# Performance work log

Measured on AMD Instinct MI355X. Metric: run time of the kernel, lower is better.

Reference implementation:

```python
import jax, jax.numpy as jnp
import numpy as np

N_NODES = 50000
N_EDGES = 800000
NODE_FEAT = 176
EDGE_FEAT = 4
HIDDEN = 64
LAYERS = 4
LN_EPS = 1e-5


def setup_inputs() -> dict:
    key = jax.random.key(0)
    ks = jax.random.split(key, 20)
    H, H2, Hh = HIDDEN, HIDDEN * 2, HIDDEN // 2
    inp = {
        "x": jax.random.normal(ks[0], (N_NODES, NODE_FEAT), jnp.float32),
        "edge_index": jax.random.randint(ks[1], (2, N_EDGES), 0, N_NODES, jnp.int64),
        "edge_attr": jax.random.normal(ks[2], (N_EDGES, EDGE_FEAT), jnp.float32),
        # input projection
        "in_w": jax.random.normal(ks[3], (NODE_FEAT, H), jnp.float32) * 0.05,
        "in_b": jnp.zeros((H,), jnp.float32),
        # per-layer GINEConv params (stacked over LAYERS)
        "edge_w": jax.random.normal(ks[4], (LAYERS, EDGE_FEAT, H), jnp.float32) * 0.1,
        "edge_b": jnp.zeros((LAYERS, H), jnp.float32),
        "mlp_w1": jax.random.normal(ks[5], (LAYERS, H, H2), jnp.float32) * 0.05,
        "mlp_b1": jnp.zeros((LAYERS, H2), jnp.float32),
        "mlp_w2": jax.random.normal(ks[6], (LAYERS, H2, H), jnp.float32) * 0.05,
        "mlp_b2": jnp.zeros((LAYERS, H), jnp.float32),
        "ln_g": jnp.ones((LAYERS, H), jnp.float32),
        "ln_b": jnp.zeros((LAYERS, H), jnp.float32),
        "reg_w1": jax.random.normal(ks[7], (H, Hh), jnp.float32) * 0.1,
        "reg_b1": jnp.zeros((Hh,), jnp.float32),
        "reg_w2": jax.random.normal(ks[8], (Hh, 1), jnp.float32) * 0.1,
        "reg_b2": jnp.zeros((1,), jnp.float32),
    }
    return inp


def _layernorm(z, g, b):
    mu = jnp.mean(z, axis=-1, keepdims=True)
    var = jnp.mean((z - mu) ** 2, axis=-1, keepdims=True)
    return g * (z - mu) * jax.lax.rsqrt(var + LN_EPS) + b


def reference(x, edge_index, edge_attr, in_w, in_b, edge_w, edge_b,
              mlp_w1, mlp_b1, mlp_w2, mlp_b2, ln_g, ln_b,
              reg_w1, reg_b1, reg_w2, reg_b2):
    src, dst = edge_index[0], edge_index[1]
    h = x @ in_w + in_b  # [N, H]
    for l in range(LAYERS):
        e = edge_attr @ edge_w[l] + edge_b[l]              # [E, H] edge projection
        msg = jax.nn.relu(h[src] + e)                      # gather + relu
        aggr = jax.ops.segment_sum(msg, dst, num_segments=h.shape[0])  # scatter-add
        z = h + aggr                                       # (1+eps)*x_i + aggr, eps=0
        z = jax.nn.relu(z @ mlp_w1[l] + mlp_b1[l]) @ mlp_w2[l] + mlp_b2[l]
        h = jax.nn.relu(_layernorm(z, ln_g[l], ln_b[l]))
    g = jnp.sum(h, axis=0)                                 # global_add_pool, single graph
    out = jax.nn.relu(g @ reg_w1 + reg_b1) @ reg_w2 + reg_b2
    return out.squeeze()
```

## Files before the change

kernel.cpp:

```cpp
#include <hip/hip_runtime.h>

#define N_NODES 50000
#define N_EDGES 800000
#define NODE_FEAT 176
#define HIDDEN 64
#define LN_EPS 1e-5f
#define SCAN_NB 49

typedef short bf16x8 __attribute__((ext_vector_type(8)));
typedef float f32x4 __attribute__((ext_vector_type(4)));
typedef long long ll2 __attribute__((ext_vector_type(2)));

__device__ __forceinline__ unsigned short f2bf(float f) {
    unsigned int u = __float_as_uint(f);
    u += 0x7FFFu + ((u >> 16) & 1u);
    return (unsigned short)(u >> 16);
}
__device__ __forceinline__ int pack2(float lo, float hi) {
    return (int)(((unsigned)f2bf(hi) << 16) | (unsigned)f2bf(lo));
}
__device__ __forceinline__ float bf2f(unsigned short s) {
    return __uint_as_float(((unsigned int)s) << 16);
}

#if __has_builtin(__builtin_amdgcn_cvt_pk_fp8_f32) && __has_builtin(__builtin_amdgcn_cvt_f32_fp8)
#define HW_FP8 1
#endif

__device__ __forceinline__ unsigned char f2fp8(float f) {
#ifdef HW_FP8
    return (unsigned char)(__builtin_amdgcn_cvt_pk_fp8_f32(f, f, 0, false) & 0xff);
#else
    unsigned u = __float_as_uint(f);
    unsigned s = (u >> 24) & 0x80u;
    float a = fabsf(f);
    if (a >= 448.f) return (unsigned char)(s | 0x7E);
    if (a < 0.0078125f) {
        int m = (int)fmaf(a, 512.0f, 0.5f);
        return (unsigned char)(s | (m > 7 ? 7 : m));
    }
    unsigned au = u & 0x7fffffffu;
    au += 0x7ffffu + ((au >> 20) & 1u);
    int e8 = (int)(au >> 23) - 120;
    if (e8 <= 0) {
        int m = (int)fmaf(__uint_as_float(au), 512.0f, 0.5f);
        return (unsigned char)(s | (m > 7 ? 7 : m));
    }
    if (e8 > 15) return (unsigned char)(s | 0x7E);
    return (unsigned char)(s | (e8 << 3) | ((au >> 20) & 7));
#endif
}
__device__ __forceinline__ float fp82f(int b) {
#ifdef HW_FP8
    return __builtin_amdgcn_cvt_f32_fp8(b & 0xff, 0);
#else
    int s = (b >> 7) & 1, e = (b >> 3) & 15, m = b & 7;
    float v = e ? __uint_as_float(((unsigned)(e + 120) << 23) | ((unsigned)m << 20))
                : (float)m * 0.001953125f;
    return s ? -v : v;
#endif
}

__device__ __forceinline__ float wave_sum64(float v) {
#pragma unroll
    for (int o = 32; o > 0; o >>= 1) v += __shfl_xor(v, o);
    return v;
}
__device__ __forceinline__ float sum16(float v) {
#pragma unroll
    for (int o = 8; o > 0; o >>= 1) v += __shfl_xor(v, o);
    return v;
}

__global__ __launch_bounds__(256) void k_wprep(const float* __restrict__ in_w,
                                               const float* __restrict__ w1,
                                               const float* __restrict__ w2,
                                               unsigned short* __restrict__ fin,
                                               unsigned short* __restrict__ f1,
                                               unsigned short* __restrict__ f2,
                                               int* __restrict__ cnt) {
    int t = blockIdx.x * 256 + threadIdx.x;
    if (t < N_NODES) cnt[t] = 0;
    if (t < 12288) {
        int e = t;
        int r = e & 7, lane = (e >> 3) & 63, j = (e >> 9) & 3, s = e >> 11;
        int k = s * 32 + ((lane >> 4) << 3) + r;
        int n = (j << 4) + (lane & 15);
        fin[e] = (k < NODE_FEAT) ? f2bf(in_w[k * 64 + n]) : (unsigned short)0;
    } else if (t < 12288 + 32768) {
        int e = t - 12288;
        int L = e >> 13, e2 = e & 8191;
        int r = e2 & 7, lane = (e2 >> 3) & 63, j = (e2 >> 9) & 7, s = (e2 >> 12) & 1;
        int k = s * 32 + ((lane >> 4) << 3) + r;
        int n = (j << 4) + (lane & 15);
        f1[e] = f2bf(w1[L * 8192 + k * 128 + n]);
    } else if (t < 12288 + 32768 + 32768) {
        int e = t - 45056;
        int L = e >> 13, e2 = e & 8191;
        int r = e2 & 7, lane = (e2 >> 3) & 63, j = (e2 >> 9) & 3, s = (e2 >> 11) & 3;
        int k = s * 32 + ((lane >> 4) << 3) + r;
        int n = (j << 4) + (lane & 15);
        f2[e] = f2bf(w2[L * 8192 + k * 64 + n]);
    }
}

__global__ __launch_bounds__(256) void k_inproj_mfma(const float* __restrict__ x,
                                                     const unsigned short* __restrict__ wfrag,
                                                     const float* __restrict__ in_b,
                                                     unsigned short* __restrict__ hb,
                                                     unsigned char* __restrict__ hf8) {
    __shared__ unsigned short lw[12288];
    const int tid = threadIdx.x;
    {
        const bf16x8* src = (const bf16x8*)wfrag;
        bf16x8* dst = (bf16x8*)lw;
        for (int i = tid; i < 1536; i += 256) dst[i] = src[i];
    }
    __syncthreads();
    const int wv = tid >> 6, lane = tid & 63;
    const int lrow = lane & 15, lgrp = lane >> 4;
    float ib[4];
#pragma unroll
    for (int j = 0; j < 4; ++j) ib[j] = in_b[16 * j + lrow];
    const int nwaves = gridDim.x * 4;
    for (int tile = blockIdx.x * 4 + wv; tile < 3125; tile += nwaves) {
        const int m0 = tile * 16;
        f32x4 acc[4];
#pragma unroll
        for (int j = 0; j < 4; ++j) acc[j] = (f32x4){ib[j], ib[j], ib[j], ib[j]};
#pragma unroll
        for (int s = 0; s < 6; ++s) {
            const int kbase = s * 32 + lgrp * 8;
            bf16x8 a;
            if (kbase < NODE_FEAT) {
                const float* p = x + (size_t)(m0 + lrow) * NODE_FEAT + kbase;
                float4 fa = *(const float4*)p;
                float4 fb = *(const float4*)(p + 4);
                a[0] = (short)f2bf(fa.x); a[1] = (short)f2bf(fa.y);
                a[2] = (short)f2bf(fa.z); a[3] = (short)f2bf(fa.w);
                a[4] = (short)f2bf(fb.x); a[5] = (short)f2bf(fb.y);
                a[6] = (short)f2bf(fb.z); a[7] = (short)f2bf(fb.w);
            } else {
                a = (bf16x8){0, 0, 0, 0, 0, 0, 0, 0};
            }
#pragma unroll
            for (int j = 0; j < 4; ++j) {
                bf16x8 b = *(const bf16x8*)&lw[((s * 4 + j) * 64 + lane) * 8];
                acc[j] = __builtin_amdgcn_mfma_f32_16x16x32_bf16(a, b, acc[j], 0, 0, 0);
            }
        }
#pragma unroll
        for (int j = 0; j < 4; ++j) {
            const int col = 16 * j + lrow;
#pragma unroll
            for (int r = 0; r < 4; ++r) {
                const int node = m0 + lgrp * 4 + r;
                float v = acc[j][r];
                __builtin_nontemporal_store(f2bf(v), &hb[(size_t)node * 64 + col]);
                hf8[(size_t)node * 64 + col] = f2fp8(v);
            }
        }
    }
}

__global__ __launch_bounds__(256) void k_hist(const int* __restrict__ ei,
                                              int* __restrict__ cnt,
                                              int* __restrict__ erank) {
    const int tid = blockIdx.x * 256 + threadIdx.x;
#pragma unroll
    for (int k = 0; k < 6; ++k) {
        int e = tid + k * 131072;
        erank[e] = atomicAdd(&cnt[ei[N_EDGES + e]], 1);
    }
    {
        int e = tid + 6 * 131072;
        if (e < N_EDGES) erank[e] = atomicAdd(&cnt[ei[N_EDGES + e]], 1);
    }
}

__global__ __launch_bounds__(256) void k_scan_part(const int* __restrict__ cnt,
                                                   int* __restrict__ blksum) {
    const int b = blockIdx.x, t = threadIdx.x;
    const int base = b * 1024 + t * 4;
    int s = 0;
#pragma unroll
    for (int i = 0; i < 4; ++i) {
        int idx = base + i;
        if (idx < N_NODES) s += cnt[idx];
    }
#pragma unroll
    for (int o = 32; o > 0; o >>= 1) s += __shfl_xor(s, o);
    __shared__ int wt[4];
    if ((t & 63) == 0) wt[t >> 6] = s;
    __syncthreads();
    if (t == 0) blksum[b] = wt[0] + wt[1] + wt[2] + wt[3];
}

__global__ __launch_bounds__(256) void k_scan_add(const int* __restrict__ cnt,
                                                  const int* __restrict__ blksum,
                                                  int* __restrict__ row_ptr) {
    const int b = blockIdx.x, t = threadIdx.x;
    __shared__ int boff_s;
    if (t < 64) {
        int v = (t < SCAN_NB) ? blksum[t] : 0;
        int incl = v;
#pragma unroll
        for (int o = 1; o < 64; o <<= 1) {
            int u = __shfl_up(incl, o);
            if (t >= o) incl += u;
        }
        if (t == b) boff_s = incl - v;
        if (b == 0 && t == 63) row_ptr[N_NODES] = incl;
    }
    __syncthreads();
    const int base = b * 1024 + t * 4;
    int c[4];
    int tsum = 0;
#pragma unroll
    for (int i = 0; i < 4; ++i) {
        int idx = base + i;
        c[i] = (idx < N_NODES) ? cnt[idx] : 0;
        tsum += c[i];
    }
    int incl = tsum;
#pragma unroll
    for (int o = 1; o < 64; o <<= 1) {
        int u = __shfl_up(incl, o);
        if ((t & 63) >= o) incl += u;
    }
    __shared__ int wt[4];
    const int wv = t >> 6;
    if ((t & 63) == 63) wt[wv] = incl;
    __syncthreads();
    int run = boff_s + (incl - tsum);
    for (int w = 0; w < wv; ++w) run += wt[w];
#pragma unroll
    for (int i = 0; i < 4; ++i) {
        int idx = base + i;
        if (idx < N_NODES) row_ptr[idx] = run;
        run += c[i];
    }
}

__global__ __launch_bounds__(256) void k_scatter(const int* __restrict__ ei,
                                                 const float4* __restrict__ ea,
                                                 const int* __restrict__ row_ptr,
                                                 const int* __restrict__ erank,
                                                 int4* __restrict__ rec) {
    int e = blockIdx.x * 256 + threadIdx.x;
    if (e >= N_EDGES) return;
    int d = ei[N_EDGES + e];
    float4 a = ea[e];
    int4 r;
    r.x = pack2(a.x, a.y);
    r.y = pack2(a.z, a.w);
    r.z = ei[e];
    r.w = 0;
    rec[row_ptr[d] + erank[e]] = r;
}

__global__ __launch_bounds__(256) void k_aggr(const unsigned short* __restrict__ hb_in,
                                              const unsigned char* __restrict__ hf8_in,
                                              unsigned short* __restrict__ zb,
                                              const int* __restrict__ row_ptr,
                                              const int4* __restrict__ rec,
                                              const float* __restrict__ ew,
                                              const float* __restrict__ eb) {
    const int wv = threadIdx.x >> 6, lane = threadIdx.x & 63;
    const int node = blockIdx.x * 4 + wv;
    const float ew0 = ew[0 * 64 + lane], ew1 = ew[1 * 64 + lane];
    const float ew2 = ew[2 * 64 + lane], ew3 = ew[3 * 64 + lane];
    const float ebl = eb[lane];
    const int beg = __builtin_amdgcn_readfirstlane(row_ptr[node]);
    const int end = __builtin_amdgcn_readfirstlane(row_ptr[node + 1]);
    float acc = bf2f(__builtin_nontemporal_load(&hb_in[(size_t)node * 64 + lane]));
    const int nb = (end - beg) >> 3;
    int i = beg;
    ll2 ra[8];
    if (nb > 0) {
#pragma unroll
        for (int t = 0; t < 8; ++t)
            ra[t] = __builtin_nontemporal_load((const ll2*)(rec + i + t));
    }
    for (int k = 0; k < nb; ++k) {
        ll2 rb[8];
        if (k + 1 < nb) {
#pragma unroll
            for (int t = 0; t < 8; ++t)
                rb[t] = __builtin_nontemporal_load((const ll2*)(rec + i + 8 + t));
        }
        int d0[8], d1[8], sx[8];
#pragma unroll
        for (int t = 0; t < 8; ++t) {
            d0[t] = __builtin_amdgcn_readfirstlane((int)(ra[t][0] & 0xffffffffLL));
            d1[t] = __builtin_amdgcn_readfirstlane((int)(ra[t][0] >> 32));
            sx[t] = __builtin_amdgcn_readfirstlane((int)(ra[t][1] & 0xffffffffLL));
        }
        float gg[8];
#pragma unroll
        for (int t = 0; t < 8; ++t)
            gg[t] = fp82f(hf8_in[((size_t)sx[t] << 6) + lane]);
#pragma unroll
        for (int t = 0; t < 8; ++t) {
            float a0 = __uint_as_float((unsigned)d0[t] << 16);
            float a1 = __uint_as_float((unsigned)d0[t] & 0xffff0000u);
            float a2 = __uint_as_float((unsigned)d1[t] << 16);
            float a3 = __uint_as_float((unsigned)d1[t] & 0xffff0000u);
            float v = fmaf(a0, ew0, fmaf(a1, ew1, fmaf(a2, ew2, fmaf(a3, ew3, ebl))));
            acc += fmaxf(v + gg[t], 0.0f);
        }
        if (k + 1 < nb) {
#pragma unroll
            for (int t = 0; t < 8; ++t) ra[t] = rb[t];
        }
        i += 8;
    }
    if (i < end) {
        const int n = end - i;
        int d0[8], d1[8], sx[8];
#pragma unroll
        for (int t = 0; t < 8; ++t) {
            int idx = i + ((t < n) ? t : (n - 1));
            ll2 r = __builtin_nontemporal_load((const ll2*)(rec + idx));
            d0[t] = __builtin_amdgcn_readfirstlane((int)(r[0] & 0xffffffffLL));
            d1[t] = __builtin_amdgcn_readfirstlane((int)(r[0] >> 32));
            sx[t] = __builtin_amdgcn_readfirstlane((int)(r[1] & 0xffffffffLL));
        }
        float gg[8];
#pragma unroll
        for (int t = 0; t < 8; ++t)
            gg[t] = fp82f(hf8_in[((size_t)sx[t] << 6) + lane]);
#pragma unroll
        for (int t = 0; t < 8; ++t) {
            float m = (t < n) ? 1.0f : 0.0f;
            float a0 = __uint_as_float((unsigned)d0[t] << 16);
            float a1 = __uint_as_float((unsigned)d0[t] & 0xffff0000u);
            float a2 = __uint_as_float((unsigned)d1[t] << 16);
            float a3 = __uint_as_float((unsigned)d1[t] & 0xffff0000u);
            float v = fmaf(a0, ew0, fmaf(a1, ew1, fmaf(a2, ew2, fmaf(a3, ew3, ebl))));
            acc += m * fmaxf(v + gg[t], 0.0f);
        }
    }
    __builtin_nontemporal_store(f2bf(acc), &zb[(size_t)node * 64 + lane]);
}

__global__ __launch_bounds__(256) void k_mlp_mfma(const unsigned short* __restrict__ zb,
                                                  unsigned short* __restrict__ hb_out,
                                                  unsigned char* __restrict__ hf8_out,
                                                  const unsigned short* __restrict__ f1,
                                                  const unsigned short* __restrict__ f2,
                                                  const float* __restrict__ b1,
                                                  const float* __restrict__ b2,
                                                  const float* __restrict__ lng,
                                                  const float* __restrict__ lnb) {
    __shared__ unsigned short w1f[8192];
    __shared__ unsigned short w2f[8192];
    __shared__ unsigned short z1s[4][2048];
    const int tid = threadIdx.x;
    {
        const bf16x8* s1 = (const bf16x8*)f1;
        const bf16x8* s2 = (const bf16x8*)f2;
        bf16x8* d1 = (bf16x8*)w1f;
        bf16x8* d2 = (bf16x8*)w2f;
        for (int i = tid; i < 1024; i += 256) { d1[i] = s1[i]; d2[i] = s2[i]; }
    }
    __syncthreads();
    const int wv = tid >> 6, lane = tid & 63;
    const int lrow = lane & 15, lgrp = lane >> 4;
    unsigned short* zs = z1s[wv];
    float bb1[8], bb2[4], g4[4], be4[4];
#pragma unroll
    for (int j = 0; j < 8; ++j) bb1[j] = b1[16 * j + lrow];
#pragma unroll
    for (int j = 0; j < 4; ++j) {
        bb2[j] = b2[16 * j + lrow];
        g4[j] = lng[16 * j + lrow];
        be4[j] = lnb[16 * j + lrow];
    }
    const int nwaves = gridDim.x * 4;
    for (int tile = blockIdx.x * 4 + wv; tile < 3125; tile += nwaves) {
        const int m0 = tile * 16;
        f32x4 acc1[8];
#pragma unroll
        for (int j = 0; j < 8; ++j) acc1[j] = (f32x4){bb1[j], bb1[j], bb1[j], bb1[j]};
#pragma unroll
        for (int s = 0; s < 2; ++s) {
            const int kbase = s * 32 + lgrp * 8;
            bf16x8 a = *(const bf16x8*)&zb[(size_t)(m0 + lrow) * 64 + kbase];
#pragma unroll
            for (int j = 0; j < 8; ++j) {
                bf16x8 b = *(const bf16x8*)&w1f[((s * 8 + j) * 64 + lane) * 8];
                acc1[j] = __builtin_amdgcn_mfma_f32_16x16x32_bf16(a, b, acc1[j], 0, 0, 0);
            }
        }
#pragma unroll
        for (int j = 0; j < 8; ++j) {
            const int col = 16 * j + lrow;
#pragma unroll
            for (int r = 0; r < 4; ++r) {
                const int row = lgrp * 4 + r;
                const int idx = (row * 128 + col) ^ ((row & 7) << 3);
                zs[idx] = f2bf(fmaxf(acc1[j][r], 0.0f));
            }
        }
        f32x4 acc2[4];
#pragma unroll
        for (int j = 0; j < 4; ++j) acc2[j] = (f32x4){bb2[j], bb2[j], bb2[j], bb2[j]};
#pragma unroll
        for (int s = 0; s < 4; ++s) {
            const int kbase = s * 32 + lgrp * 8;
            const int idx = (lrow * 128 + kbase) ^ ((lrow & 7) << 3);
            bf16x8 a = *(const bf16x8*)&zs[idx];
#pragma unroll
            for (int j = 0; j < 4; ++j) {
                bf16x8 b = *(const bf16x8*)&w2f[((s * 4 + j) * 64 + lane) * 8];
                acc2[j] = __builtin_amdgcn_mfma_f32_16x16x32_bf16(a, b, acc2[j], 0, 0, 0);
            }
        }
#pragma unroll
        for (int r = 0; r < 4; ++r) {
            float sum = acc2[0][r] + acc2[1][r] + acc2[2][r] + acc2[3][r];
            sum = sum16(sum);
            const float mu = sum * (1.0f / 64.0f);
            float sq = 0.0f;
#pragma unroll
            for (int j = 0; j < 4; ++j) {
                float d = acc2[j][r] - mu;
                sq = fmaf(d, d, sq);
            }
            sq = sum16(sq);
            const float rstd = rsqrtf(sq * (1.0f / 64.0f) + LN_EPS);
            const int node = m0 + lgrp * 4 + r;
#pragma unroll
            for (int j = 0; j < 4; ++j) {
                const int col = 16 * j + lrow;
                float d = acc2[j][r] - mu;
                float hn = fmaxf(fmaf(g4[j] * d, rstd, be4[j]), 0.0f);
                __builtin_nontemporal_store(f2bf(hn), &hb_out[(size_t)node * 64 + col]);
                hf8_out[(size_t)node * 64 + col] = f2fp8(hn);
            }
        }
    }
}

__global__ __launch_bounds__(256) void k_pool(const unsigned short* __restrict__ hb,
                                              float* __restrict__ gpart) {
    __shared__ float red[256];
    const int tid = threadIdx.x;
    const int lane = tid & 63;
    float part = 0.0f;
    for (int i = blockIdx.x * 4 + (tid >> 6); i < N_NODES; i += gridDim.x * 4)
        part += bf2f(hb[(size_t)i * 64 + lane]);
    red[tid] = part;
    __syncthreads();
    if (tid < 64) {
        gpart[blockIdx.x * 64 + tid] = red[tid] + red[tid + 64] + red[tid + 128] + red[tid + 192];
    }
}

__global__ __launch_bounds__(64) void k_reg(const float* __restrict__ gpart,
                                            const float* __restrict__ w1,
                                            const float* __restrict__ b1,
                                            const float* __restrict__ w2,
                                            const float* __restrict__ b2,
                                            float* __restrict__ out) {
    const int j = threadIdx.x;
    float gj = 0.0f;
    for (int b = 0; b < 256; ++b) gj += gpart[b * 64 + j];
    __shared__ float gs[64];
    gs[j] = gj;
    __syncthreads();
    const int jm = j & 31;
    float acc = b1[jm];
#pragma unroll 8
    for (int k = 0; k < 64; ++k) {
        float gk = gs[k];
        acc = fmaf(gk, w1[k * 32 + jm], acc);
    }
    float contrib = (j < 32) ? fmaxf(acc, 0.0f) * w2[jm] : 0.0f;
    float s = wave_sum64(contrib);
    if (j == 0) out[0] = s + b2[0];
}

extern "C" void kernel_launch(void* const* d_in, const int* in_sizes, int n_in,
                              void* d_out, int out_size, void* d_ws, size_t ws_size,
                              hipStream_t stream) {
    const float* x      = (const float*)d_in[0];
    const int*   ei     = (const int*)d_in[1];
    const float* ea     = (const float*)d_in[2];
    const float* in_w   = (const float*)d_in[3];
    const float* in_b   = (const float*)d_in[4];
    const float* edge_w = (const float*)d_in[5];
    const float* edge_b = (const float*)d_in[6];
    const float* mlp_w1 = (const float*)d_in[7];
    const float* mlp_b1 = (const float*)d_in[8];
    const float* mlp_w2 = (const float*)d_in[9];
    const float* mlp_b2 = (const float*)d_in[10];
    const float* ln_g   = (const float*)d_in[11];
    const float* ln_b   = (const float*)d_in[12];
    const float* reg_w1 = (const float*)d_in[13];
    const float* reg_b1 = (const float*)d_in[14];
    const float* reg_w2 = (const float*)d_in[15];
    const float* reg_b2 = (const float*)d_in[16];

    char* ws = (char*)d_ws;
    unsigned short* hb0     = (unsigned short*)ws; ws += (size_t)N_NODES * 64 * 2;
    unsigned short* hb1     = (unsigned short*)ws; ws += (size_t)N_NODES * 64 * 2;
    unsigned short* zb      = (unsigned short*)ws; ws += (size_t)N_NODES * 64 * 2;
    unsigned char*  hf8_0   = (unsigned char*)ws;  ws += (size_t)N_NODES * 64;
    unsigned char*  hf8_1   = (unsigned char*)ws;  ws += (size_t)N_NODES * 64;
    int4*           rec     = (int4*)ws;           ws += (size_t)N_EDGES * 16;
    unsigned short* fin     = (unsigned short*)ws; ws += 12288 * 2;
    unsigned short* f1      = (unsigned short*)ws; ws += 32768 * 2;
    unsigned short* f2      = (unsigned short*)ws; ws += 32768 * 2;
    int*            erank   = (int*)ws;            ws += (size_t)N_EDGES * 4;
    int*            row_ptr = (int*)ws;            ws += (size_t)(N_NODES + 1) * 4;
    int*            cnt     = (int*)ws;            ws += (size_t)N_NODES * 4;
    int*            blksum  = (int*)ws;            ws += SCAN_NB * 4;
    float*          gpart   = (float*)ws;          ws += 256 * 64 * 4;
    float*          outf    = (float*)d_out;

    const int eb_blocks = (N_EDGES + 255) / 256;

    k_wprep<<<304, 256, 0, stream>>>(in_w, mlp_w1, mlp_w2, fin, f1, f2, cnt);

    k_hist<<<512, 256, 0, stream>>>(ei, cnt, erank);
    k_scan_part<<<SCAN_NB, 256, 0, stream>>>(cnt, blksum);
    k_scan_add<<<SCAN_NB, 256, 0, stream>>>(cnt, blksum, row_ptr);
    k_scatter<<<eb_blocks, 256, 0, stream>>>(ei, (const float4*)ea, row_ptr, erank, rec);

    k_inproj_mfma<<<512, 256, 0, stream>>>(x, fin, in_b, hb0, hf8_0);

    unsigned short* hbA = hb0;
    unsigned short* hbB = hb1;
    unsigned char*  hfA = hf8_0;
    unsigned char*  hfB = hf8_1;
    for (int l = 0; l < 4; ++l) {
        k_aggr<<<N_NODES / 4, 256, 0, stream>>>(hbA, hfA, zb, row_ptr, rec,
                                                edge_w + l * 4 * 64,
                                                edge_b + l * 64);
        k_mlp_mfma<<<768, 256, 0, stream>>>(zb, hbB, hfB,
                                            f1 + l * 8192, f2 + l * 8192,
                                            mlp_b1 + l * 128, mlp_b2 + l * 64,
                                            ln_g + l * 64, ln_b + l * 64);
        unsigned short* tb = hbA; hbA = hbB; hbB = tb;
        unsigned char*  tf = hfA; hfA = hfB; hfB = tf;
    }

    k_pool<<<256, 256, 0, stream>>>(hbA, gpart);
    k_reg<<<1, 64, 0, stream>>>(gpart, reg_w1, reg_b1, reg_w2, reg_b2, outf);
}
```

Measured before the change: 284.3 us.

## Replace global-atomic CSR build with per-block LDS histograms and offset matrix

The edge bucketing by destination moves from global atomics (histogram plus per-edge rank) to 64 blocks, each building LDS histograms over four node ranges for its edge chunk. A 64xN count matrix is scanned to produce per-block write offsets, and a second pass scatters records using LDS atomics for the local rank. This removes contended global atomics and the erank array. In exchange, only 64 blocks run, each edge chunk is scanned eight times in total, and the scan kernels now read and write large count and offset matrices.

```diff
diff --git a/kernel.cpp b/kernel.cpp
--- a/kernel.cpp
+++ b/kernel.cpp
@@ -6,6 +6,9 @@
 #define HIDDEN 64
 #define LN_EPS 1e-5f
 #define SCAN_NB 49
+#define NBC 64
+#define CHUNK 12500
+#define RNG 12500
 
 typedef short bf16x8 __attribute__((ext_vector_type(8)));
 typedef float f32x4 __attribute__((ext_vector_type(4)));
@@ -77,10 +80,8 @@
                                                const float* __restrict__ w2,
                                                unsigned short* __restrict__ fin,
                                                unsigned short* __restrict__ f1,
-                                               unsigned short* __restrict__ f2,
-                                               int* __restrict__ cnt) {
+                                               unsigned short* __restrict__ f2) {
     int t = blockIdx.x * 256 + threadIdx.x;
-    if (t < N_NODES) cnt[t] = 0;
     if (t < 12288) {
         int e = t;
         int r = e & 7, lane = (e >> 3) & 63, j = (e >> 9) & 3, s = e >> 11;
@@ -163,31 +164,47 @@
     }
 }
 
-__global__ __launch_bounds__(256) void k_hist(const int* __restrict__ ei,
-                                              int* __restrict__ cnt,
-                                              int* __restrict__ erank) {
-    const int tid = blockIdx.x * 256 + threadIdx.x;
-#pragma unroll
-    for (int k = 0; k < 6; ++k) {
-        int e = tid + k * 131072;
-        erank[e] = atomicAdd(&cnt[ei[N_EDGES + e]], 1);
-    }
-    {
-        int e = tid + 6 * 131072;
-        if (e < N_EDGES) erank[e] = atomicAdd(&cnt[ei[N_EDGES + e]], 1);
-    }
-}
-
-__global__ __launch_bounds__(256) void k_scan_part(const int* __restrict__ cnt,
+__global__ __launch_bounds__(256) void k_cnt(const int* __restrict__ ei,
+                                             unsigned short* __restrict__ cmat) {
+    __shared__ int h[RNG];
+    const int b = blockIdx.x, t = threadIdx.x;
+    const int e0 = b * CHUNK;
+    unsigned short* crow = cmat + (size_t)b * N_NODES;
+    for (int r = 0; r < 4; ++r) {
+        const int lo = r * RNG;
+        for (int i = t; i < RNG; i += 256) h[i] = 0;
+        __syncthreads();
+        for (int i = t; i < CHUNK; i += 256) {
+            int d = ei[N_EDGES + e0 + i];
+            unsigned dr = (unsigned)(d - lo);
+            if (dr < (unsigned)RNG) atomicAdd(&h[dr], 1);
+        }
+        __syncthreads();
+        for (int i = t; i < RNG; i += 256) crow[lo + i] = (unsigned short)h[i];
+        __syncthreads();
+    }
+}
+
+__global__ __launch_bounds__(256) void k_scan_part(const unsigned short* __restrict__ cmat,
+                                                   int* __restrict__ cnttot,
                                                    int* __restrict__ blksum) {
     const int b = blockIdx.x, t = threadIdx.x;
     const int base = b * 1024 + t * 4;
-    int s = 0;
+    int c[4] = {0, 0, 0, 0};
+    for (int bb = 0; bb < NBC; ++bb) {
+        const unsigned short* row = cmat + (size_t)bb * N_NODES;
+#pragma unroll
+        for (int i = 0; i < 4; ++i) {
+            int idx = base + i;
+            if (idx < N_NODES) c[i] += row[idx];
+        }
+    }
 #pragma unroll
     for (int i = 0; i < 4; ++i) {
         int idx = base + i;
-        if (idx < N_NODES) s += cnt[idx];
-    }
+        if (idx < N_NODES) cnttot[idx] = c[i];
+    }
+    int s = c[0] + c[1] + c[2] + c[3];
 #pragma unroll
     for (int o = 32; o > 0; o >>= 1) s += __shfl_xor(s, o);
     __shared__ int wt[4];
@@ -196,9 +213,11 @@
     if (t == 0) blksum[b] = wt[0] + wt[1] + wt[2] + wt[3];
 }
 
-__global__ __launch_bounds__(256) void k_scan_add(const int* __restrict__ cnt,
+__global__ __launch_bounds__(256) void k_scan_add(const int* __restrict__ cnttot,
                                                   const int* __restrict__ blksum,
-                                                  int* __restrict__ row_ptr) {
+                                                  const unsigned short* __restrict__ cmat,
+                                                  int* __restrict__ row_ptr,
+                                                  int* __restrict__ omat) {
     const int b = blockIdx.x, t = threadIdx.x;
     __shared__ int boff_s;
     if (t < 64) {
@@ -219,7 +238,7 @@
 #pragma unroll
     for (int i = 0; i < 4; ++i) {
         int idx = base + i;
-        c[i] = (idx < N_NODES) ? cnt[idx] : 0;
+        c[i] = (idx < N_NODES) ? cnttot[idx] : 0;
         tsum += c[i];
     }
     int incl = tsum;
@@ -234,29 +253,57 @@
     __syncthreads();
     int run = boff_s + (incl - tsum);
     for (int w = 0; w < wv; ++w) run += wt[w];
+    int rp[4];
 #pragma unroll
     for (int i = 0; i < 4; ++i) {
         int idx = base + i;
+        rp[i] = run;
         if (idx < N_NODES) row_ptr[idx] = run;
         run += c[i];
     }
-}
-
-__global__ __launch_bounds__(256) void k_scatter(const int* __restrict__ ei,
-                                                 const float4* __restrict__ ea,
-                                                 const int* __restrict__ row_ptr,
-                                                 const int* __restrict__ erank,
-                                                 int4* __restrict__ rec) {
-    int e = blockIdx.x * 256 + threadIdx.x;
-    if (e >= N_EDGES) return;
-    int d = ei[N_EDGES + e];
-    float4 a = ea[e];
-    int4 r;
-    r.x = pack2(a.x, a.y);
-    r.y = pack2(a.z, a.w);
-    r.z = ei[e];
-    r.w = 0;
-    rec[row_ptr[d] + erank[e]] = r;
+    int accq[4] = {0, 0, 0, 0};
+    for (int bb = 0; bb < NBC; ++bb) {
+        const size_t ro = (size_t)bb * N_NODES;
+#pragma unroll
+        for (int i = 0; i < 4; ++i) {
+            int idx = base + i;
+            if (idx < N_NODES) {
+                omat[ro + idx] = rp[i] + accq[i];
+                accq[i] += cmat[ro + idx];
+            }
+        }
+    }
+}
+
+__global__ __launch_bounds__(256) void k_scatter2(const int* __restrict__ ei,
+                                                  const float4* __restrict__ ea,
+                                                  const int* __restrict__ omat,
+                                                  int4* __restrict__ rec) {
+    __shared__ int h[RNG];
+    const int b = blockIdx.x, t = threadIdx.x;
+    const int e0 = b * CHUNK;
+    const int* om = omat + (size_t)b * N_NODES;
+    for (int r = 0; r < 4; ++r) {
+        const int lo = r * RNG;
+        for (int i = t; i < RNG; i += 256) h[i] = 0;
+        __syncthreads();
+        for (int i = t; i < CHUNK; i += 256) {
+            const int e = e0 + i;
+            int d = ei[N_EDGES + e];
+            unsigned dr = (unsigned)(d - lo);
+            if (dr < (unsigned)RNG) {
+                int lr = atomicAdd(&h[dr], 1);
+                float4 a = ea[e];
+                int4 rr;
+                rr.x = pack2(a.x, a.y);
+                rr.y = pack2(a.z, a.w);
+                rr.z = ei[e];
+                rr.w = 0;
+                rec[om[d] + lr] = rr;
+            }
+        }
+        __syncthreads();
+    }
 }
 
 __global__ __launch_bounds__(256) void k_aggr(const unsigned short* __restrict__ hb_in,
@@ -513,21 +560,20 @@
     unsigned short* fin     = (unsigned short*)ws; ws += 12288 * 2;
     unsigned short* f1      = (unsigned short*)ws; ws += 32768 * 2;
     unsigned short* f2      = (unsigned short*)ws; ws += 32768 * 2;
-    int*            erank   = (int*)ws;            ws += (size_t)N_EDGES * 4;
+    unsigned short* cmat    = (unsigned short*)ws; ws += (size_t)NBC * N_NODES * 2;
+    int*            omat    = (int*)ws;            ws += (size_t)NBC * N_NODES * 4;
     int*            row_ptr = (int*)ws;            ws += (size_t)(N_NODES + 1) * 4;
     int*            cnt     = (int*)ws;            ws += (size_t)N_NODES * 4;
     int*            blksum  = (int*)ws;            ws += SCAN_NB * 4;
     float*          gpart   = (float*)ws;          ws += 256 * 64 * 4;
     float*          outf    = (float*)d_out;
 
-    const int eb_blocks = (N_EDGES + 255) / 256;
-
-    k_wprep<<<304, 256, 0, stream>>>(in_w, mlp_w1, mlp_w2, fin, f1, f2, cnt);
-
-    k_hist<<<512, 256, 0, stream>>>(ei, cnt, erank);
-    k_scan_part<<<SCAN_NB, 256, 0, stream>>>(cnt, blksum);
-    k_scan_add<<<SCAN_NB, 256, 0, stream>>>(cnt, blksum, row_ptr);
-    k_scatter<<<eb_blocks, 256, 0, stream>>>(ei, (const float4*)ea, row_ptr, erank, rec);
+    k_wprep<<<304, 256, 0, stream>>>(in_w, mlp_w1, mlp_w2, fin, f1, f2);
+
+    k_cnt<<<NBC, 256, 0, stream>>>(ei, cmat);
+    k_scan_part<<<SCAN_NB, 256, 0, stream>>>(cmat, cnt, blksum);
+    k_scan_add<<<SCAN_NB, 256, 0, stream>>>(cnt, blksum, cmat, row_ptr, omat);
+    k_scatter2<<<NBC, 256, 0, stream>>>(ei, (const float4*)ea, omat, rec);
 
     k_inproj_mfma<<<512, 256, 0, stream>>>(x, fin, in_b, hb0, hf8_0);
 
```

Measured after the change: 475.4 us. +67.2%, slower.
